# Kernel tuning notes

Measured on AMD Instinct MI355X. Metric: run time of the kernel, lower is better.

Reference implementation:

```python
import jax, jax.numpy as jnp
import numpy as np

VOCAB = 50257
CUTOFF = (10000, 50000, 50257)  # cutoff + [vocab_size] per __init__
D = 1024
B, T = 2, 1024
HEAD_SZ = CUTOFF[0] + 2  # cutoff[0] + n_tail_clusters


def setup_inputs() -> dict:
    key = jax.random.key(0)
    ks = jax.random.split(key, 7)
    def xavier(k, shp):
        # xavier_uniform as in init_weights
        bound = np.sqrt(6.0 / (shp[0] + shp[1])).astype(np.float32)
        return jax.random.uniform(k, shp, dtype=jnp.float32, minval=-bound, maxval=bound)
    return {
        "input": jax.random.normal(ks[0], (B, T, D), dtype=jnp.float32),
        "target": jax.random.randint(ks[1], (B, T), 0, VOCAB),
        "head_w": xavier(ks[2], (HEAD_SZ, D)),              # [10002, 1024]
        "t0_a": xavier(ks[3], (D, D)),                       # [1024, 1024]
        "t0_b": xavier(ks[4], (CUTOFF[1] - CUTOFF[0], D)),   # [40000, 1024]
        "t1_a": xavier(ks[5], (D // 4, D)),                  # [256, 1024]
        "t1_b": xavier(ks[6], (CUTOFF[2] - CUTOFF[1], D // 4)),  # [207, 256]
    }


def reference(input, target, head_w, t0_a, t0_b, t1_a, t1_b):
    # Faithful jax version of AdaptiveSoftmax.get_log_prob (eval mode, dropout=0).
    # Torch updates log_probs[idxs, start:end] only for rows whose target lies in
    # cluster i (leaving other rows zero); we express the same gather->small GEMM
    # chain->log_softmax->prior-add->scatter via masked writes (jit-friendly).
    bsz, length, dim = input.shape
    xi = input.reshape(-1, dim)                     # [N, D]
    tgt = target.reshape(-1)                        # [N]

    head_lp = jax.nn.log_softmax(xi @ head_w.T, axis=1)        # [N, HEAD_SZ]
    tail_priors = head_lp[:, CUTOFF[0] - 1:HEAD_SZ - 1]        # [N, 2]

    log_probs = jnp.zeros((xi.shape[0], VOCAB), dtype=input.dtype)
    log_probs = log_probs.at[:, :HEAD_SZ].set(head_lp)

    tails = ((t0_a, t0_b), (t1_a, t1_b))
    for i, (wa, wb) in enumerate(tails):
        lo, hi = CUTOFF[i], CUTOFF[i + 1]
        mask = (tgt >= lo) & (tgt < hi)                        # [N]
        # Linear(D, D//4**i) -> Linear(D//4**i, hi-lo), then log_softmax + prior
        tail_lp = jax.nn.log_softmax((xi @ wa.T) @ wb.T, axis=1) + tail_priors[:, i:i + 1]
        log_probs = log_probs.at[:, lo:hi].set(
            jnp.where(mask[:, None], tail_lp, log_probs[:, lo:hi]))
    return log_probs.reshape(bsz, length, VOCAB)
```

## Files before the change

### kernel.cpp

```cpp
#include <hip/hip_runtime.h>

typedef unsigned short u16;
typedef unsigned int u32;
typedef __attribute__((ext_vector_type(4))) float f32x4;
typedef __bf16 bf16x8 __attribute__((ext_vector_type(8)));
typedef __attribute__((ext_vector_type(8))) unsigned short u16x8;

__device__ __forceinline__ u16 f2bf(float x) {
    u32 u = __builtin_bit_cast(u32, x);
    u += 0x7FFFu + ((u >> 16) & 1u);
    return (u16)(u >> 16);
}
__device__ __forceinline__ float bf2f(u16 u) {
    return __builtin_bit_cast(float, ((u32)u) << 16);
}
__device__ __forceinline__ void gld_lds16(void* lds, const void* g) {
    __builtin_amdgcn_global_load_lds(
        (const __attribute__((address_space(1))) void*)g,
        (__attribute__((address_space(3))) void*)lds, 16, 0, 0);
}

__device__ __forceinline__ size_t pack_base_tail(long row) {
    return (size_t)row * 100514 + 59936 - ((row * 2) & 7);
}
__device__ __forceinline__ size_t pack_base_head(long row) {
    return (size_t)row * 100514 + 20480 - ((row * 2) & 7);
}

__device__ __forceinline__ void cvt_range(const float* __restrict__ src,
                                          u16* __restrict__ dst, int n,
                                          int bloc, int nb) {
    int i0 = bloc * 1024 + threadIdx.x * 4;
    int stride = nb * 1024;
    if (src) {
        for (int i = i0; i < n; i += stride) {
            float4 v = *(const float4*)(src + i);
            ushort4 o;
            o.x = f2bf(v.x); o.y = f2bf(v.y); o.z = f2bf(v.z); o.w = f2bf(v.w);
            *(ushort4*)(dst + i) = o;
        }
    } else {
        ushort4 z = {0, 0, 0, 0};
        for (int i = i0; i < n; i += stride) *(ushort4*)(dst + i) = z;
    }
}

__global__ __launch_bounds__(256) void cvt1(const float* __restrict__ x,
                                            const float* __restrict__ hw,
                                            const float* __restrict__ t0a,
                                            const float* __restrict__ t1a,
                                            const float* __restrict__ t1b,
                                            const int* __restrict__ tgt,
                                            u16* __restrict__ XI, u16* __restrict__ HW,
                                            u16* __restrict__ TAB, u16* __restrict__ T1B,
                                            int* __restrict__ rowlist, int* __restrict__ cntbuf) {
    int b = blockIdx.x;
    if (b < 80)       { cvt_range(x,   XI,            2097152,  b,       80);  return; }
    if (b < 472)      { cvt_range(hw,  HW,            10242048, b - 80,  392); return; }
    if (b < 512)      { cvt_range(t0a, TAB,           1048576,  b - 472, 40);  return; }
    if (b < 522)      { cvt_range(t1a, TAB + 1048576, 262144,   b - 512, 10);  return; }
    if (b < 526)      { cvt_range(t1b, T1B,           65792,    b - 522, 4);   return; }
    if (b < 536)      { cvt_range(0,   HW + 10242048, 243712,   b - 526, 10);  return; }
    __shared__ int cs[257];
    int t = threadIdx.x;
    int cnt_local = 0;
    int mk[8];
#pragma unroll
    for (int k = 0; k < 8; k++) {
        int tg = tgt[t * 8 + k];
        mk[k] = (tg >= 10000 && tg < 50000) ? 1 : 0;
        cnt_local += mk[k];
    }
    cs[t + 1] = cnt_local;
    __syncthreads();
    if (t == 0) {
        cs[0] = 0;
        for (int i = 1; i <= 256; i++) cs[i] += cs[i - 1];
        cntbuf[0] = cs[256];
        cntbuf[1] = (cs[256] + 255) & ~255;
    }
    __syncthreads();
    int cnt = cs[256];
    int offm = cs[t];
    int offu = cnt + (t * 8 - cs[t]);
#pragma unroll
    for (int k = 0; k < 8; k++) {
        if (mk[k]) rowlist[offm++] = t * 8 + k;
        else       rowlist[offu++] = t * 8 + k;
    }
}

__global__ __launch_bounds__(256) void proj_cvt(const u16* __restrict__ A,
                                                const u16* __restrict__ B,
                                                u16* __restrict__ Cb,
                                                const float* __restrict__ t0b,
                                                u16* __restrict__ T0B) {
    int b = blockIdx.x;
    if (b >= 160) {
        if (b < 1724) cvt_range(t0b, T0B, 40960000, b - 160, 1564);
        else          cvt_range(0, T0B + 40960000, 196608, b - 1724, 8);
        return;
    }
    __shared__ u16 lA[128 * 32];
    __shared__ u16 lB[128 * 32];
    const int tid = threadIdx.x;
    const int lane = tid & 63, wv = tid >> 6;
    const int m0 = (b & 15) * 128, n0 = (b >> 4) * 128;

    const u16* gA0 = A + (size_t)(m0 + (tid >> 2)) * 1024 + (tid & 3) * 8;
    const u16* gB0 = B + (size_t)(n0 + (tid >> 2)) * 1024 + (tid & 3) * 8;
    char* dA = (char*)lA + wv * 1024;
    char* dB = (char*)lB + wv * 1024;

    f32x4 acc[4][4] = {};
    const int wm = wv >> 1, wn = wv & 1;
    const int lr = lane & 15;
    const int lk = (lane >> 4) * 8;

    for (int kt = 0; kt < 1024; kt += 32) {
        __syncthreads();
        gld_lds16(dA, gA0);
        gld_lds16(dA + 4096, gA0 + 64 * 1024);
        gld_lds16(dB, gB0);
        gld_lds16(dB + 4096, gB0 + 64 * 1024);
        gA0 += 32; gB0 += 32;
        __syncthreads();

        bf16x8 af[4], bfr[4];
#pragma unroll
        for (int i = 0; i < 4; i++) {
            af[i]  = *(const bf16x8*)(lA + (wm * 64 + i * 16 + lr) * 32 + lk);
            bfr[i] = *(const bf16x8*)(lB + (wn * 64 + i * 16 + lr) * 32 + lk);
        }
#pragma unroll
        for (int i = 0; i < 4; i++)
#pragma unroll
            for (int j = 0; j < 4; j++)
                acc[i][j] = __builtin_amdgcn_mfma_f32_16x16x32_bf16(af[i], bfr[j], acc[i][j], 0, 0, 0);
    }

    const int cr = (lane >> 4) * 4;
    const int cc = lane & 15;
#pragma unroll
    for (int i = 0; i < 4; i++) {
        int rbase = m0 + wm * 64 + i * 16 + cr;
#pragma unroll
        for (int j = 0; j < 4; j++) {
            int c = n0 + wn * 64 + j * 16 + cc;
#pragma unroll
            for (int q = 0; q < 4; q++)
                Cb[(size_t)(rbase + q) * 1280 + c] = f2bf(acc[i][j][q]);
        }
    }
}

template <int TAIL>
__global__ __launch_bounds__(512, 1) void gemm256p(const u16* __restrict__ A,
                                                   const u16* __restrict__ B,
                                                   u16* __restrict__ outpk,
                                                   const int* __restrict__ rowlist,
                                                   const int* __restrict__ cntbuf,
                                                   float* __restrict__ part) {
    const int NY = TAIL ? 157 : 40;
    const int l = blockIdx.y * 8 + blockIdx.x;
    const int w = (l & 7) * NY + (l >> 3);
    const int m0 = (w & 7) * 256, n0 = (w >> 3) * 256;
    if (TAIL) { if (m0 >= cntbuf[1]) return; }
    __shared__ u16 lds[65536];
    const int tid = threadIdx.x;
    const int lane = tid & 63, wv = tid >> 6;
    const int wm = wv >> 2, wn = wv & 3;
    const int lr = lane & 15, hi = lane >> 4;

    const int rp = ((tid >> 7) << 4) + (tid & 15);
    const int kp = ((tid >> 4) & 7) * 8;
    const u16 *pA[2][2], *pB[2][2];
#pragma unroll
    for (int h = 0; h < 2; h++) {
#pragma unroll
        for (int c = 0; c < 2; c++) {
            int row = h * 128 + rp + c * 64;
            if (TAIL) pA[h][c] = A + (size_t)rowlist[m0 + row] * 1280 + kp;
            else      pA[h][c] = A + (size_t)(m0 + row) * 1024 + kp;
            pB[h][c] = B + (size_t)(n0 + row) * 1024 + kp;
        }
    }

    f32x4 acc[8][4] = {};
    bf16x8 Bf[4][2], Af[2][2];

    auto stA = [&](int s, int h, int t) {
        u16* d = lds + s * 16384 + h * 8192 + tid * 8;
        int ko = t * 64;
        gld_lds16(d, pA[h][0] + ko);
        gld_lds16(d + 4096, pA[h][1] + ko);
    };
    auto stB = [&](int s, int h, int t) {
        u16* d = lds + 32768 + s * 16384 + h * 8192 + tid * 8;
        int ko = t * 64;
        gld_lds16(d, pB[h][0] + ko);
        gld_lds16(d + 4096, pB[h][1] + ko);
    };
    auto rdB = [&](int s) {
        const u16* base = lds + 32768 + s * 16384 + (wn >> 1) * 8192 + (wn & 1) * 4096 + hi * 128 + lr * 8;
#pragma unroll
        for (int j = 0; j < 4; j++)
#pragma unroll
            for (int ks = 0; ks < 2; ks++)
                Bf[j][ks] = *(const bf16x8*)(base + j * 1024 + ks * 512);
    };
    auto rdA = [&](int s, int p) {
        const u16* base = lds + s * 16384 + wm * 8192 + p * 2048 + hi * 128 + lr * 8;
#pragma unroll
        for (int m = 0; m < 2; m++)
#pragma unroll
            for (int ks = 0; ks < 2; ks++)
                Af[m][ks] = *(const bf16x8*)(base + m * 1024 + ks * 512);
    };
    auto mf = [&](int p) {
        __builtin_amdgcn_s_setprio(1);
#pragma unroll
        for (int m = 0; m < 2; m++)
#pragma unroll
            for (int j = 0; j < 4; j++)
#pragma unroll
                for (int ks = 0; ks < 2; ks++)
                    acc[p * 2 + m][j] = __builtin_amdgcn_mfma_f32_16x16x32_bf16(
                        Af[m][ks], Bf[j][ks], acc[p * 2 + m][j], 0, 0, 0);
        __builtin_amdgcn_s_setprio(0);
    };

#define BAR_()   __builtin_amdgcn_s_barrier()
#define LGKM0_() do { asm volatile("s_waitcnt lgkmcnt(0)" ::: "memory"); \
                      __builtin_amdgcn_sched_barrier(0); } while (0)
#define VM4_()   asm volatile("s_waitcnt vmcnt(4)" ::: "memory")
#define VM0_()   asm volatile("s_waitcnt vmcnt(0)" ::: "memory")

    stA(0, 0, 0); stA(0, 1, 0); stB(0, 0, 0); stB(0, 1, 0);
    VM0_();
    stB(1, 0, 1); stB(1, 1, 1);
    BAR_();

    auto iter = [&](int t0, bool full) {
        rdB(0); rdA(0, 0);
        stA(1, 0, t0 + 1);
        BAR_(); LGKM0_(); mf(0); BAR_();
        rdA(0, 1);
        stA(1, 1, t0 + 1);
        __builtin_amdgcn_sched_barrier(0);
        if (full) stB(0, 0, t0 + 2);
        BAR_(); LGKM0_(); mf(1); BAR_();
        rdA(0, 2);
        if (full) stB(0, 1, t0 + 2);
        BAR_(); LGKM0_(); mf(2); BAR_();
        rdA(0, 3);
        if (full) { VM4_(); } else { VM0_(); }
        BAR_(); LGKM0_(); mf(3); BAR_();
        rdB(1); rdA(1, 0);
        if (full) stA(0, 0, t0 + 2);
        BAR_(); LGKM0_(); mf(0); BAR_();
        rdA(1, 1);
        if (full) { stA(0, 1, t0 + 2);
                    __builtin_amdgcn_sched_barrier(0);
                    stB(1, 0, t0 + 3); }
        BAR_(); LGKM0_(); mf(1); BAR_();
        rdA(1, 2);
        if (full) stB(1, 1, t0 + 3);
        BAR_(); LGKM0_(); mf(2); BAR_();
        rdA(1, 3);
        if (full) VM4_();
        BAR_(); LGKM0_(); mf(3); BAR_();
    };
#pragma unroll 1
    for (int i = 0; i < 7; i++) iter(2 * i, true);
    iter(14, false);

#undef BAR_
#undef LGKM0_
#undef VM4_
#undef VM0_

    const int cr = hi * 4, cc = lr;
    const int climit = TAIL ? 40000 : 10002;
    const int pstride = TAIL ? 628 : 160;
#pragma unroll
    for (int m = 0; m < 8; m++) {
#pragma unroll
        for (int q = 0; q < 4; q++) {
            int r = m0 + wm * 128 + m * 16 + cr + q;
            long orow = TAIL ? rowlist[r] : r;
            size_t base = TAIL ? pack_base_tail(orow) : pack_base_head(orow);
            u16* dst = outpk + base + n0 + wn * 64 + cc;
            float s = 0.f;
#pragma unroll
            for (int j = 0; j < 4; j++) {
                float v = acc[m][j][q];
                dst[j * 16] = f2bf(v);
                int col = n0 + wn * 64 + j * 16 + cc;
                s += (col < climit) ? __expf(v) : 0.f;
            }
            s += __shfl_xor(s, 1); s += __shfl_xor(s, 2);
            s += __shfl_xor(s, 4); s += __shfl_xor(s, 8);
            if (cc == 0) part[(size_t)r * pstride + (n0 >> 6) + wn] = s;
        }
    }
}

__global__ __launch_bounds__(256) void norm_all(float* __restrict__ out,
                                                const int* __restrict__ tgt,
                                                const int* __restrict__ rowlist,
                                                const int* __restrict__ cntbuf,
                                                const float* __restrict__ PARTH,
                                                const float* __restrict__ PART,
                                                const u16* __restrict__ proj,
                                                const u16* __restrict__ t1b) {
    const int b = blockIdx.x, tid = threadIdx.x;
    const int cnt = cntbuf[0];
    const long row = rowlist[b];
    __shared__ float red[4];
    __shared__ float pr[256];
    __shared__ float lg[257];
    float* p0 = out + (size_t)row * 50257;

    float s = (tid < 160) ? PARTH[(size_t)row * 160 + tid] : 0.f;
#pragma unroll
    for (int o = 32; o; o >>= 1) s += __shfl_xor(s, o);
    if ((tid & 63) == 0) red[tid >> 6] = s;
    __syncthreads();
    float logZh = __logf(red[0] + red[1] + red[2] + red[3]);
    const u16* pkh = (const u16*)out + pack_base_head(row);
    float prior0 = bf2f(pkh[9999]) - logZh;
    float l1 = bf2f(pkh[10000]) - logZh;
    float l2 = bf2f(pkh[10001]) - logZh;
    for (int k = 0; k < 5; k++) {
        int c0 = k * 2048 + tid * 8;
        if (c0 + 8 <= 10002) {
            u16x8 xv = *(const u16x8*)(pkh + c0);
#pragma unroll
            for (int z = 0; z < 8; z++) p0[c0 + z] = bf2f(xv[z]) - logZh;
        } else if (c0 < 10002) {
            for (int z = 0; c0 + z < 10002; z++) p0[c0 + z] = bf2f(pkh[c0 + z]) - logZh;
        }
    }
    __syncthreads();

    float* p = p0 + 10000;
    if (b < cnt) {
        float s2 = 0.f;
        for (int c = tid; c < 628; c += 256) s2 += PART[(size_t)b * 628 + c];
#pragma unroll
        for (int o = 32; o; o >>= 1) s2 += __shfl_xor(s2, o);
        if ((tid & 63) == 0) red[tid >> 6] = s2;
        __syncthreads();
        float Aa = __logf(red[0] + red[1] + red[2] + red[3]) - prior0;
        const u16* src = (const u16*)out + pack_base_tail(row);
        for (int k = 0; k < 5; k++) {
            float v[4][8];
#pragma unroll
            for (int g = 0; g < 4; g++) {
                int o = 2048 * g + tid * 8;
                if (o < 8000) {
                    u16x8 xv = *(const u16x8*)(src + 8000 * k + o);
#pragma unroll
                    for (int z = 0; z < 8; z++) v[g][z] = bf2f(xv[z]);
                }
            }
            __syncthreads();
#pragma unroll
            for (int g = 0; g < 4; g++) {
                int o = 2048 * g + tid * 8;
                if (o < 8000) {
                    int e = 8000 * k + o;
#pragma unroll
                    for (int z = 0; z < 8; z++) p[e + z] = v[g][z] - Aa;
                }
            }
            __syncthreads();
        }
    } else {
        for (int e = tid; e < 40000; e += 256) p[e] = 0.f;
        if (tid == 0) { p[0] = l1; p[1] = l2; }
        __syncthreads();
    }

    float* p5 = p0 + 50000;
    int t = tgt[row];
    if (t < 50000) {
        for (int c = tid; c < 257; c += 256) p5[c] = 0.f;
        return;
    }
    pr[tid] = bf2f(proj[(size_t)row * 1280 + 1024 + tid]);
    __syncthreads();
    for (int c = tid; c < 257; c += 256) {
        const u16* wp = t1b + c * 256;
        float acc = 0.f;
        for (int k = 0; k < 256; k++) acc += bf2f(wp[k]) * pr[k];
        lg[c] = acc;
    }
    __syncthreads();
    float s1 = 0.f;
    for (int c = tid; c < 257; c += 256) s1 += __expf(lg[c]);
#pragma unroll
    for (int o = 32; o; o >>= 1) s1 += __shfl_xor(s1, o);
    if ((tid & 63) == 0) red[tid >> 6] = s1;
    __syncthreads();
    float A = __logf(red[0] + red[1] + red[2] + red[3]) - l1;
    for (int c = tid; c < 257; c += 256) p5[c] = lg[c] - A;
}

#define OFF_XI    0UL
#define OFF_HEADW 4194304UL
#define OFF_TAB   25165824UL
#define OFF_T0B   27787264UL
#define OFF_T1B   110100480UL
#define OFF_PROJ  110232064UL
#define OFF_PART  115474944UL
#define OFF_PARTH 120619520UL
#define OFF_MAP   121930240UL
#define OFF_CNT   121938432UL

extern "C" void kernel_launch(void* const* d_in, const int* in_sizes, int n_in,
                              void* d_out, int out_size, void* d_ws, size_t ws_size,
                              hipStream_t stream) {
    const float* x   = (const float*)d_in[0];
    const int*   tgt = (const int*)d_in[1];
    const float* hw  = (const float*)d_in[2];
    const float* t0a = (const float*)d_in[3];
    const float* t0b = (const float*)d_in[4];
    const float* t1a = (const float*)d_in[5];
    const float* t1b = (const float*)d_in[6];
    float* out = (float*)d_out;
    char* ws = (char*)d_ws;

    u16* XI     = (u16*)(ws + OFF_XI);
    u16* HW     = (u16*)(ws + OFF_HEADW);
    u16* TAB    = (u16*)(ws + OFF_TAB);
    u16* T0B    = (u16*)(ws + OFF_T0B);
    u16* T1B    = (u16*)(ws + OFF_T1B);
    u16* PROJ   = (u16*)(ws + OFF_PROJ);
    float* PART = (float*)(ws + OFF_PART);
    float* PARTH = (float*)(ws + OFF_PARTH);
    int* MAP    = (int*)(ws + OFF_MAP);
    int* CNT    = (int*)(ws + OFF_CNT);

    cvt1<<<537, 256, 0, stream>>>(x, hw, t0a, t1a, t1b, tgt, XI, HW, TAB, T1B, MAP, CNT);

    proj_cvt<<<1732, 256, 0, stream>>>(XI, TAB, PROJ, t0b, T0B);

    gemm256p<0><<<dim3(8, 40), 512, 0, stream>>>(XI, HW, (u16*)d_out, nullptr, nullptr, PARTH);

    gemm256p<1><<<dim3(8, 157), 512, 0, stream>>>(PROJ, T0B, (u16*)d_out, MAP, CNT, PART);

    norm_all<<<2048, 256, 0, stream>>>(out, tgt, MAP, CNT, PARTH, PART, PROJ, T1B);
}
```

Before: 537.4 us.

## Fuse projection GEMM, head GEMM and t0_b conversion into one launch

Replaces the separate proj_cvt kernel and the head gemm256p launch with a single fused2 kernel. Its grid gives 40 block-rows to the projection GEMM on the 256x256 pipelined tile path, 320 to the head GEMM, and the remaining blocks to fp32-to-bf16 conversion of t0_b. The intent is to cut one launch and let the bandwidth-bound conversion overlap the compute-bound GEMMs. The projection now uses larger 256-wide tiles, so it gets fewer blocks, and the shared one-block-per-CU launch bounds may reduce occupancy for the conversion blocks.

```diff
diff --git a/kernel.cpp b/kernel.cpp
--- a/kernel.cpp
+++ b/kernel.cpp
@@ -32,6 +32,23 @@
                                           int bloc, int nb) {
     int i0 = bloc * 1024 + threadIdx.x * 4;
     int stride = nb * 1024;
+    if (src) {
+        for (int i = i0; i < n; i += stride) {
+            float4 v = *(const float4*)(src + i);
+            ushort4 o;
+            o.x = f2bf(v.x); o.y = f2bf(v.y); o.z = f2bf(v.z); o.w = f2bf(v.w);
+            *(ushort4*)(dst + i) = o;
+        }
+    } else {
+        ushort4 z = {0, 0, 0, 0};
+        for (int i = i0; i < n; i += stride) *(ushort4*)(dst + i) = z;
+    }
+}
+__device__ __forceinline__ void cvt_range512(const float* __restrict__ src,
+                                             u16* __restrict__ dst, int n,
+                                             int bloc, int nb) {
+    int i0 = bloc * 2048 + threadIdx.x * 4;
+    int stride = nb * 2048;
     if (src) {
         for (int i = i0; i < n; i += stride) {
             float4 v = *(const float4*)(src + i);
@@ -90,82 +107,27 @@
     }
 }
 
-__global__ __launch_bounds__(256) void proj_cvt(const u16* __restrict__ A,
-                                                const u16* __restrict__ B,
-                                                u16* __restrict__ Cb,
-                                                const float* __restrict__ t0b,
-                                                u16* __restrict__ T0B) {
-    int b = blockIdx.x;
-    if (b >= 160) {
-        if (b < 1724) cvt_range(t0b, T0B, 40960000, b - 160, 1564);
-        else          cvt_range(0, T0B + 40960000, 196608, b - 1724, 8);
+__global__ __launch_bounds__(512, 1) void fused2(const u16* __restrict__ XI,
+                                                 const u16* __restrict__ TAB,
+                                                 const u16* __restrict__ HW,
+                                                 u16* __restrict__ PROJ,
+                                                 u16* __restrict__ outpk,
+                                                 float* __restrict__ parth,
+                                                 const float* __restrict__ t0b,
+                                                 u16* __restrict__ T0B) {
+    const int y = blockIdx.y;
+    if (y >= 45) {
+        int bc = (y - 45) * 8 + blockIdx.x;
+        if (bc < 568) cvt_range512(t0b, T0B, 40960000, bc, 568);
+        else          cvt_range512(0, T0B + 40960000, 196608, bc - 568, 8);
         return;
     }
-    __shared__ u16 lA[128 * 32];
-    __shared__ u16 lB[128 * 32];
-    const int tid = threadIdx.x;
-    const int lane = tid & 63, wv = tid >> 6;
-    const int m0 = (b & 15) * 128, n0 = (b >> 4) * 128;
-
-    const u16* gA0 = A + (size_t)(m0 + (tid >> 2)) * 1024 + (tid & 3) * 8;
-    const u16* gB0 = B + (size_t)(n0 + (tid >> 2)) * 1024 + (tid & 3) * 8;
-    char* dA = (char*)lA + wv * 1024;
-    char* dB = (char*)lB + wv * 1024;
-
-    f32x4 acc[4][4] = {};
-    const int wm = wv >> 1, wn = wv & 1;
-    const int lr = lane & 15;
-    const int lk = (lane >> 4) * 8;
-
-    for (int kt = 0; kt < 1024; kt += 32) {
-        __syncthreads();
-        gld_lds16(dA, gA0);
-        gld_lds16(dA + 4096, gA0 + 64 * 1024);
-        gld_lds16(dB, gB0);
-        gld_lds16(dB + 4096, gB0 + 64 * 1024);
-        gA0 += 32; gB0 += 32;
-        __syncthreads();
-
-        bf16x8 af[4], bfr[4];
-#pragma unroll
-        for (int i = 0; i < 4; i++) {
-            af[i]  = *(const bf16x8*)(lA + (wm * 64 + i * 16 + lr) * 32 + lk);
-            bfr[i] = *(const bf16x8*)(lB + (wn * 64 + i * 16 + lr) * 32 + lk);
-        }
-#pragma unroll
-        for (int i = 0; i < 4; i++)
-#pragma unroll
-            for (int j = 0; j < 4; j++)
-                acc[i][j] = __builtin_amdgcn_mfma_f32_16x16x32_bf16(af[i], bfr[j], acc[i][j], 0, 0, 0);
-    }
-
-    const int cr = (lane >> 4) * 4;
-    const int cc = lane & 15;
-#pragma unroll
-    for (int i = 0; i < 4; i++) {
-        int rbase = m0 + wm * 64 + i * 16 + cr;
-#pragma unroll
-        for (int j = 0; j < 4; j++) {
-            int c = n0 + wn * 64 + j * 16 + cc;
-#pragma unroll
-            for (int q = 0; q < 4; q++)
-                Cb[(size_t)(rbase + q) * 1280 + c] = f2bf(acc[i][j][q]);
-        }
-    }
-}
-
-template <int TAIL>
-__global__ __launch_bounds__(512, 1) void gemm256p(const u16* __restrict__ A,
-                                                   const u16* __restrict__ B,
-                                                   u16* __restrict__ outpk,
-                                                   const int* __restrict__ rowlist,
-                                                   const int* __restrict__ cntbuf,
-                                                   float* __restrict__ part) {
-    const int NY = TAIL ? 157 : 40;
-    const int l = blockIdx.y * 8 + blockIdx.x;
+    const bool proj = y < 5;
+    const int NY = proj ? 5 : 40;
+    const int l = (proj ? y : y - 5) * 8 + blockIdx.x;
     const int w = (l & 7) * NY + (l >> 3);
     const int m0 = (w & 7) * 256, n0 = (w >> 3) * 256;
-    if (TAIL) { if (m0 >= cntbuf[1]) return; }
+    const u16* B = proj ? TAB : HW;
     __shared__ u16 lds[65536];
     const int tid = threadIdx.x;
     const int lane = tid & 63, wv = tid >> 6;
@@ -180,8 +142,7 @@
 #pragma unroll
         for (int c = 0; c < 2; c++) {
             int row = h * 128 + rp + c * 64;
-            if (TAIL) pA[h][c] = A + (size_t)rowlist[m0 + row] * 1280 + kp;
-            else      pA[h][c] = A + (size_t)(m0 + row) * 1024 + kp;
+            pA[h][c] = XI + (size_t)(m0 + row) * 1024 + kp;
             pB[h][c] = B + (size_t)(n0 + row) * 1024 + kp;
         }
     }
@@ -281,6 +242,166 @@
 #undef VM0_
 
     const int cr = hi * 4, cc = lr;
+    if (proj) {
+#pragma unroll
+        for (int m = 0; m < 8; m++)
+#pragma unroll
+            for (int q = 0; q < 4; q++) {
+                int r = m0 + wm * 128 + m * 16 + cr + q;
+#pragma unroll
+                for (int j = 0; j < 4; j++)
+                    PROJ[(size_t)r * 1280 + n0 + wn * 64 + j * 16 + cc] = f2bf(acc[m][j][q]);
+            }
+        return;
+    }
+#pragma unroll
+    for (int m = 0; m < 8; m++) {
+#pragma unroll
+        for (int q = 0; q < 4; q++) {
+            int r = m0 + wm * 128 + m * 16 + cr + q;
+            u16* dst = outpk + pack_base_head((long)r) + n0 + wn * 64 + cc;
+            float s = 0.f;
+#pragma unroll
+            for (int j = 0; j < 4; j++) {
+                float v = acc[m][j][q];
+                dst[j * 16] = f2bf(v);
+                int col = n0 + wn * 64 + j * 16 + cc;
+                s += (col < 10002) ? __expf(v) : 0.f;
+            }
+            s += __shfl_xor(s, 1); s += __shfl_xor(s, 2);
+            s += __shfl_xor(s, 4); s += __shfl_xor(s, 8);
+            if (cc == 0) parth[(size_t)r * 160 + (n0 >> 6) + wn] = s;
+        }
+    }
+}
+
+template <int TAIL>
+__global__ __launch_bounds__(512, 1) void gemm256p(const u16* __restrict__ A,
+                                                   const u16* __restrict__ B,
+                                                   u16* __restrict__ outpk,
+                                                   const int* __restrict__ rowlist,
+                                                   const int* __restrict__ cntbuf,
+                                                   float* __restrict__ part) {
+    const int NY = TAIL ? 157 : 40;
+    const int l = blockIdx.y * 8 + blockIdx.x;
+    const int w = (l & 7) * NY + (l >> 3);
+    const int m0 = (w & 7) * 256, n0 = (w >> 3) * 256;
+    if (TAIL) { if (m0 >= cntbuf[1]) return; }
+    __shared__ u16 lds[65536];
+    const int tid = threadIdx.x;
+    const int lane = tid & 63, wv = tid >> 6;
+    const int wm = wv >> 2, wn = wv & 3;
+    const int lr = lane & 15, hi = lane >> 4;
+
+    const int rp = ((tid >> 7) << 4) + (tid & 15);
+    const int kp = ((tid >> 4) & 7) * 8;
+    const u16 *pA[2][2], *pB[2][2];
+#pragma unroll
+    for (int h = 0; h < 2; h++) {
+#pragma unroll
+        for (int c = 0; c < 2; c++) {
+            int row = h * 128 + rp + c * 64;
+            if (TAIL) pA[h][c] = A + (size_t)rowlist[m0 + row] * 1280 + kp;
+            else      pA[h][c] = A + (size_t)(m0 + row) * 1024 + kp;
+            pB[h][c] = B + (size_t)(n0 + row) * 1024 + kp;
+        }
+    }
+
+    f32x4 acc[8][4] = {};
+    bf16x8 Bf[4][2], Af[2][2];
+
+    auto stA = [&](int s, int h, int t) {
+        u16* d = lds + s * 16384 + h * 8192 + tid * 8;
+        int ko = t * 64;
+        gld_lds16(d, pA[h][0] + ko);
+        gld_lds16(d + 4096, pA[h][1] + ko);
+    };
+    auto stB = [&](int s, int h, int t) {
+        u16* d = lds + 32768 + s * 16384 + h * 8192 + tid * 8;
+        int ko = t * 64;
+        gld_lds16(d, pB[h][0] + ko);
+        gld_lds16(d + 4096, pB[h][1] + ko);
+    };
+    auto rdB = [&](int s) {
+        const u16* base = lds + 32768 + s * 16384 + (wn >> 1) * 8192 + (wn & 1) * 4096 + hi * 128 + lr * 8;
+#pragma unroll
+        for (int j = 0; j < 4; j++)
+#pragma unroll
+            for (int ks = 0; ks < 2; ks++)
+                Bf[j][ks] = *(const bf16x8*)(base + j * 1024 + ks * 512);
+    };
+    auto rdA = [&](int s, int p) {
+        const u16* base = lds + s * 16384 + wm * 8192 + p * 2048 + hi * 128 + lr * 8;
+#pragma unroll
+        for (int m = 0; m < 2; m++)
+#pragma unroll
+            for (int ks = 0; ks < 2; ks++)
+                Af[m][ks] = *(const bf16x8*)(base + m * 1024 + ks * 512);
+    };
+    auto mf = [&](int p) {
+        __builtin_amdgcn_s_setprio(1);
+#pragma unroll
+        for (int m = 0; m < 2; m++)
+#pragma unroll
+            for (int j = 0; j < 4; j++)
+#pragma unroll
+                for (int ks = 0; ks < 2; ks++)
+                    acc[p * 2 + m][j] = __builtin_amdgcn_mfma_f32_16x16x32_bf16(
+                        Af[m][ks], Bf[j][ks], acc[p * 2 + m][j], 0, 0, 0);
+        __builtin_amdgcn_s_setprio(0);
+    };
+
+#define BAR_()   __builtin_amdgcn_s_barrier()
+#define LGKM0_() do { asm volatile("s_waitcnt lgkmcnt(0)" ::: "memory"); \
+                      __builtin_amdgcn_sched_barrier(0); } while (0)
+#define VM4_()   asm volatile("s_waitcnt vmcnt(4)" ::: "memory")
+#define VM0_()   asm volatile("s_waitcnt vmcnt(0)" ::: "memory")
+
+    stA(0, 0, 0); stA(0, 1, 0); stB(0, 0, 0); stB(0, 1, 0);
+    VM0_();
+    stB(1, 0, 1); stB(1, 1, 1);
+    BAR_();
+
+    auto iter = [&](int t0, bool full) {
+        rdB(0); rdA(0, 0);
+        stA(1, 0, t0 + 1);
+        BAR_(); LGKM0_(); mf(0); BAR_();
+        rdA(0, 1);
+        stA(1, 1, t0 + 1);
+        __builtin_amdgcn_sched_barrier(0);
+        if (full) stB(0, 0, t0 + 2);
+        BAR_(); LGKM0_(); mf(1); BAR_();
+        rdA(0, 2);
+        if (full) stB(0, 1, t0 + 2);
+        BAR_(); LGKM0_(); mf(2); BAR_();
+        rdA(0, 3);
+        if (full) { VM4_(); } else { VM0_(); }
+        BAR_(); LGKM0_(); mf(3); BAR_();
+        rdB(1); rdA(1, 0);
+        if (full) stA(0, 0, t0 + 2);
+        BAR_(); LGKM0_(); mf(0); BAR_();
+        rdA(1, 1);
+        if (full) { stA(0, 1, t0 + 2);
+                    __builtin_amdgcn_sched_barrier(0);
+                    stB(1, 0, t0 + 3); }
+        BAR_(); LGKM0_(); mf(1); BAR_();
+        rdA(1, 2);
+        if (full) stB(1, 1, t0 + 3);
+        BAR_(); LGKM0_(); mf(2); BAR_();
+        rdA(1, 3);
+        if (full) VM4_();
+        BAR_(); LGKM0_(); mf(3); BAR_();
+    };
+#pragma unroll 1
+    for (int i = 0; i < 7; i++) iter(2 * i, true);
+    iter(14, false);
+
+#undef BAR_
+#undef LGKM0_
+#undef VM4_
+#undef VM0_
+
+    const int cr = hi * 4, cc = lr;
     const int climit = TAIL ? 40000 : 10002;
     const int pstride = TAIL ? 628 : 160;
 #pragma unroll
@@ -445,9 +566,7 @@
 
     cvt1<<<537, 256, 0, stream>>>(x, hw, t0a, t1a, t1b, tgt, XI, HW, TAB, T1B, MAP, CNT);
 
-    proj_cvt<<<1732, 256, 0, stream>>>(XI, TAB, PROJ, t0b, T0B);
-
-    gemm256p<0><<<dim3(8, 40), 512, 0, stream>>>(XI, HW, (u16*)d_out, nullptr, nullptr, PARTH);
+    fused2<<<dim3(8, 117), 512, 0, stream>>>(XI, TAB, HW, PROJ, (u16*)d_out, PARTH, t0b, T0B);
 
     gemm256p<1><<<dim3(8, 157), 512, 0, stream>>>(PROJ, T0B, (u16*)d_out, MAP, CNT, PART);
 
```

Result: faster. 506.3 us (-5.8%).
